# Optimization experiments

Measured on AMD Instinct MI355X. Metric: run time of the kernel, lower is better.

The kernel has to match this reference:

```python
import jax, jax.numpy as jnp
import numpy as np

NEG_INF = jnp.float32(-(2.0**32) + 1.0)


def squash(z):
    # z: [B, k_max, out_units]
    sq_norm = jnp.sum(jnp.square(z), axis=-1, keepdims=True)
    scale = sq_norm / (1.0 + sq_norm) / jnp.sqrt(sq_norm + 1e-8)
    return scale * z


def setup_inputs() -> dict:
    key = jax.random.key(0)
    k1, k2, k3, k4 = jax.random.split(key, 4)
    B, L, D_IN, D_OUT, K = 1024, 200, 256, 256, 8
    behavior_embeddings = jax.random.normal(k1, (B, L, D_IN), dtype=jnp.float32)
    seq_len = jax.random.randint(k2, (B, 1), 1, L + 1, dtype=jnp.int32)
    routing_logits = jax.random.normal(k3, (1, K, L), dtype=jnp.float32)  # init_std=1.0
    bilinear_mapping_matrix = jax.random.normal(k4, (D_IN, D_OUT), dtype=jnp.float32)
    return {
        "behavior_embeddings": behavior_embeddings,
        "seq_len": seq_len,
        "routing_logits": routing_logits,
        "bilinear_mapping_matrix": bilinear_mapping_matrix,
    }


def reference(behavior_embeddings, seq_len, routing_logits, bilinear_mapping_matrix):
    ITERATION_TIMES = 3
    B, L, _ = behavior_embeddings.shape
    K = routing_logits.shape[1]

    # mask: [B, 1, L] broadcastable to [B, K, L] (same seq_len for every capsule)
    mask = jnp.arange(L)[None, None, :] < seq_len[:, :, None]

    # bilinear map is loop-invariant: [B, L, out_units]
    mapped = jnp.einsum("ble,eo->blo", behavior_embeddings, bilinear_mapping_matrix)

    logits = routing_logits  # [1, K, L]
    interest_capsules = None
    for _ in range(ITERATION_TIMES):
        logits_pad = jnp.where(mask, jnp.broadcast_to(logits, (B, K, L)), NEG_INF)
        weight = jax.nn.softmax(logits_pad, axis=-1)          # [B, K, L]
        Z = jnp.einsum("bkl,blo->bko", weight, mapped)         # [B, K, out]
        interest_capsules = squash(Z)                          # [B, K, out]
        # delta: sum over batch of capsules @ mapped^T -> [1, K, L]
        delta = jnp.einsum("bko,blo->kl", interest_capsules, mapped)[None]
        logits = logits + delta  # emulates assign_add on non-trainable B

    return interest_capsules.reshape(-1, K, interest_capsules.shape[-1])
```

## Files before the change

kernel.cpp:

```cpp
#include <hip/hip_runtime.h>
#include <cstdint>
#include <cstddef>

#define B_    1024
#define L_    200
#define DIN_  256
#define DOUT_ 256
#define K_    8
#define M_    (B_ * L_)

typedef __attribute__((ext_vector_type(8))) short bf16x8;
typedef __attribute__((ext_vector_type(4))) float f32x4;

__device__ __forceinline__ float bf2f(unsigned short u) {
  union { unsigned int i; float f; } w; w.i = ((unsigned int)u) << 16; return w.f;
}
__device__ __forceinline__ unsigned short f2bf(float f) {
  union { float f; unsigned int i; } w; w.f = f;
  unsigned int x = w.i;
  return (unsigned short)((x + 0x7fffu + ((x >> 16) & 1u)) >> 16);
}

__device__ __forceinline__ void gload16(const void* g, void* l) {
  __builtin_amdgcn_global_load_lds(
      (const __attribute__((address_space(1))) unsigned int*)g,
      (__attribute__((address_space(3))) unsigned int*)l, 16, 0, 0);
}

__global__ __launch_bounds__(256)
void wt_prep(const float* __restrict__ W, unsigned short* __restrict__ Wh,
             unsigned short* __restrict__ Wm, unsigned short* __restrict__ Wl)
{
  const int k = blockIdx.x;
  const int n = threadIdx.x;
  float x = W[k * DOUT_ + n];
  unsigned short h = f2bf(x);
  float r = x - bf2f(h);
  unsigned short m = f2bf(r);
  float r2 = r - bf2f(m);
  unsigned short l = f2bf(r2);
  const int k0b = k >> 5, quad = (k >> 3) & 3, j = k & 7;
  const int nt = n >> 4, lr = n & 15;
  const size_t idx = ((((size_t)k0b * 16 + nt) * 64) + (quad * 16 + lr)) * 8 + j;
  Wh[idx] = h;
  Wm[idx] = m;
  Wl[idx] = l;
}

__global__ __launch_bounds__(256, 3)
void gemm_mapped(const float* __restrict__ A,
                 const unsigned short* __restrict__ Wh,
                 const unsigned short* __restrict__ Wm,
                 const unsigned short* __restrict__ Wl,
                 float* __restrict__ C)
{
  const int t    = threadIdx.x;
  const int wave = t >> 6;
  const int lane = t & 63;
  const int quad = lane >> 4;
  const int lr   = lane & 15;
  const int m0   = blockIdx.x * 64 + (wave & 1) * 32;
  const int nt0  = (wave >> 1) * 8;

  __shared__ unsigned short ldsB[3 * 16 * 64 * 8];

  f32x4 acc[2][8];
  #pragma unroll
  for (int mt = 0; mt < 2; ++mt)
    #pragma unroll
    for (int nt = 0; nt < 8; ++nt)
      acc[mt][nt] = (f32x4){0.f, 0.f, 0.f, 0.f};

  bf16x8 ah[2], am[2], al[2];
  float4 Af[2][2];

  const float* ap0 = A + (size_t)(m0 + lr) * DIN_ + quad * 8;
  const float* ap1 = A + (size_t)(m0 + 16 + lr) * DIN_ + quad * 8;

#define STAGE(K0B) do { \
    const size_t _k = (size_t)(K0B) * 8192; \
    _Pragma("unroll") \
    for (int _r = 0; _r < 4; ++_r) { \
      gload16(Wh + _k + _r * 2048 + t * 8, ldsB +         _r * 2048 + t * 8); \
      gload16(Wm + _k + _r * 2048 + t * 8, ldsB +  8192 + _r * 2048 + t * 8); \
      gload16(Wl + _k + _r * 2048 + t * 8, ldsB + 16384 + _r * 2048 + t * 8); \
    } \
  } while (0)

  Af[0][0] = *(const float4*)(ap0);
  Af[0][1] = *(const float4*)(ap0 + 4);
  Af[1][0] = *(const float4*)(ap1);
  Af[1][1] = *(const float4*)(ap1 + 4);
  STAGE(0);
  asm volatile("s_waitcnt vmcnt(0)" ::: "memory");
  __syncthreads();

  for (int k0b = 0; k0b < 8; ++k0b) {
    #pragma unroll
    for (int mt = 0; mt < 2; ++mt) {
      float xs[8] = {Af[mt][0].x, Af[mt][0].y, Af[mt][0].z, Af[mt][0].w,
                     Af[mt][1].x, Af[mt][1].y, Af[mt][1].z, Af[mt][1].w};
      #pragma unroll
      for (int j = 0; j < 8; ++j) {
        unsigned short h = f2bf(xs[j]);
        float r = xs[j] - bf2f(h);
        unsigned short mm = f2bf(r);
        float r2 = r - bf2f(mm);
        unsigned short ll = f2bf(r2);
        ah[mt][j] = (short)h; am[mt][j] = (short)mm; al[mt][j] = (short)ll;
      }
    }
    if (k0b < 7) {
      const int ko = (k0b + 1) * 32;
      Af[0][0] = *(const float4*)(ap0 + ko);
      Af[0][1] = *(const float4*)(ap0 + ko + 4);
      Af[1][0] = *(const float4*)(ap1 + ko);
      Af[1][1] = *(const float4*)(ap1 + ko + 4);
    }

#define GROUP(NT) do { \
    const unsigned short* _lb = ldsB + (size_t)((nt0 + (NT)) * 64 + lane) * 8; \
    bf16x8 Bh_ = *(const bf16x8*)(_lb); \
    bf16x8 Bm_ = *(const bf16x8*)(_lb + 8192); \
    bf16x8 Bl_ = *(const bf16x8*)(_lb + 16384); \
    f32x4 c0 = acc[0][NT], c1 = acc[1][NT]; \
    c0 = __builtin_amdgcn_mfma_f32_16x16x32_bf16(ah[0], Bh_, c0, 0, 0, 0); \
    c1 = __builtin_amdgcn_mfma_f32_16x16x32_bf16(ah[1], Bh_, c1, 0, 0, 0); \
    c0 = __builtin_amdgcn_mfma_f32_16x16x32_bf16(ah[0], Bm_, c0, 0, 0, 0); \
    c1 = __builtin_amdgcn_mfma_f32_16x16x32_bf16(ah[1], Bm_, c1, 0, 0, 0); \
    c0 = __builtin_amdgcn_mfma_f32_16x16x32_bf16(am[0], Bh_, c0, 0, 0, 0); \
    c1 = __builtin_amdgcn_mfma_f32_16x16x32_bf16(am[1], Bh_, c1, 0, 0, 0); \
    c0 = __builtin_amdgcn_mfma_f32_16x16x32_bf16(ah[0], Bl_, c0, 0, 0, 0); \
    c1 = __builtin_amdgcn_mfma_f32_16x16x32_bf16(ah[1], Bl_, c1, 0, 0, 0); \
    c0 = __builtin_amdgcn_mfma_f32_16x16x32_bf16(am[0], Bm_, c0, 0, 0, 0); \
    c1 = __builtin_amdgcn_mfma_f32_16x16x32_bf16(am[1], Bm_, c1, 0, 0, 0); \
    c0 = __builtin_amdgcn_mfma_f32_16x16x32_bf16(al[0], Bh_, c0, 0, 0, 0); \
    c1 = __builtin_amdgcn_mfma_f32_16x16x32_bf16(al[1], Bh_, c1, 0, 0, 0); \
    acc[0][NT] = c0; acc[1][NT] = c1; \
  } while (0)

    GROUP(0); GROUP(1); GROUP(2); GROUP(3);
    GROUP(4); GROUP(5); GROUP(6); GROUP(7);
#undef GROUP

    __syncthreads();
    if (k0b < 7) {
      STAGE(k0b + 1);
      asm volatile("s_waitcnt vmcnt(0)" ::: "memory");
      __syncthreads();
    }
  }
#undef STAGE

  #pragma unroll
  for (int mt = 0; mt < 2; ++mt)
    #pragma unroll
    for (int nt = 0; nt < 8; ++nt)
      #pragma unroll
      for (int r = 0; r < 4; ++r) {
        int row = m0 + mt * 16 + quad * 4 + r;
        C[(size_t)row * DOUT_ + (nt0 + nt) * 16 + lr] = acc[mt][nt][r];
      }
}

#define DSCALE     67108864.0f
#define DSCALE_INV 1.4901161193847656e-8f

__global__ __launch_bounds__(256, 4)
void z_soft(const float* __restrict__ mapped,
            const float* __restrict__ rlog,
            const long long* __restrict__ accA,
            const long long* __restrict__ accB,
            const int* __restrict__ seq_len,
            float* __restrict__ caps)
{
  const int t    = threadIdx.x;
  const int lane = t & 63;
  const int wave = t >> 6;
  const int b    = blockIdx.x;
  const int len  = seq_len[b];

  __shared__ float wsmT[200][8];
  __shared__ float zred[2][8][256];
  __shared__ float sqred[4][8];

  #pragma unroll
  for (int kk = 0; kk < 2; ++kk) {
    const int k = wave * 2 + kk;
    float v[4];
    float mx = -3.4028235e38f;
    #pragma unroll
    for (int i = 0; i < 4; ++i) {
      int l = lane + 64 * i;
      float lv = -3.4028235e38f;
      if (l < len) {
        long long a = accA[(k * L_ + l) * 8] + accB[(k * L_ + l) * 8];
        lv = rlog[k * L_ + l] + (float)a * DSCALE_INV;
      }
      v[i] = lv;
      mx = fmaxf(mx, lv);
    }
    #pragma unroll
    for (int s = 1; s < 64; s <<= 1) mx = fmaxf(mx, __shfl_xor(mx, s, 64));
    float e[4]; float sum = 0.f;
    #pragma unroll
    for (int i = 0; i < 4; ++i) {
      int l = lane + 64 * i;
      e[i] = (l < len) ? __expf(v[i] - mx) : 0.f;
      sum += e[i];
    }
    #pragma unroll
    for (int s = 1; s < 64; s <<= 1) sum += __shfl_xor(sum, s, 64);
    float inv = 1.f / sum;
    #pragma unroll
    for (int i = 0; i < 4; ++i) {
      int l = lane + 64 * i;
      if (l < L_) wsmT[l][k] = e[i] * inv;
    }
  }
  __syncthreads();

  f32x4 zacc[K_];
  #pragma unroll
  for (int k = 0; k < K_; ++k) zacc[k] = (f32x4){0.f, 0.f, 0.f, 0.f};

  const float* mp = mapped + (size_t)b * (L_ * DOUT_) + lane * 4;
  for (int l = wave; l < len; l += 16) {
    int  li[4];
    bool vi[4];
    #pragma unroll
    for (int r = 0; r < 4; ++r) {
      int lr_ = l + 4 * r;
      vi[r] = (lr_ < L_);
      li[r] = vi[r] ? lr_ : (L_ - 1);
    }
    f32x4 m[4];
    #pragma unroll
    for (int r = 0; r < 4; ++r)
      m[r] = *(const f32x4*)(mp + (size_t)li[r] * DOUT_);
    #pragma unroll
    for (int r = 0; r < 4; ++r) {
      float4 w0 = *(const float4*)&wsmT[li[r]][0];
      float4 w1 = *(const float4*)&wsmT[li[r]][4];
      if (!vi[r]) {
        w0.x = w0.y = w0.z = w0.w = 0.f;
        w1.x = w1.y = w1.z = w1.w = 0.f;
      }
      zacc[0] += w0.x * m[r]; zacc[1] += w0.y * m[r];
      zacc[2] += w0.z * m[r]; zacc[3] += w0.w * m[r];
      zacc[4] += w1.x * m[r]; zacc[5] += w1.y * m[r];
      zacc[6] += w1.z * m[r]; zacc[7] += w1.w * m[r];
    }
  }

  if (wave >= 2) {
    #pragma unroll
    for (int k = 0; k < K_; ++k)
      *(f32x4*)&zred[wave - 2][k][lane * 4] = zacc[k];
  }
  __syncthreads();
  if (wave < 2) {
    #pragma unroll
    for (int k = 0; k < K_; ++k) {
      f32x4 r = *(const f32x4*)&zred[wave][k][lane * 4];
      r += zacc[k];
      *(f32x4*)&zred[wave][k][lane * 4] = r;
    }
  }
  __syncthreads();

  float z[K_];
  #pragma unroll
  for (int k = 0; k < K_; ++k) z[k] = zred[0][k][t] + zred[1][k][t];

  #pragma unroll
  for (int k = 0; k < K_; ++k) {
    float s2 = z[k] * z[k];
    #pragma unroll
    for (int s = 1; s < 64; s <<= 1) s2 += __shfl_xor(s2, s, 64);
    if (lane == 0) sqred[wave][k] = s2;
  }
  __syncthreads();
  #pragma unroll
  for (int k = 0; k < K_; ++k) {
    float sq = sqred[0][k] + sqred[1][k] + sqred[2][k] + sqred[3][k];
    float scale = sq / ((1.f + sq) * sqrtf(sq + 1e-8f));
    caps[((size_t)b * K_ + k) * DOUT_ + t] = scale * z[k];
  }
}

__global__ __launch_bounds__(256)
void delta_kernel(const float* __restrict__ mapped, const float* __restrict__ caps,
                  long long* __restrict__ accOut)
{
  const int t    = threadIdx.x;
  const int lane = t & 63;
  const int wave = t >> 6;
  const int wid  = blockIdx.x * 4 + wave;
  const int lc   = wid % 50;
  const int bc   = wid / 50;
  const int l0   = lc * 4;
  const int o4   = lane * 4;

  const float* cb = caps   + (size_t)(bc * 16) * (K_ * DOUT_) + o4;
  const float* mb = mapped + ((size_t)(bc * 16) * L_ + l0) * DOUT_ + o4;

  float acc[K_][4];
  #pragma unroll
  for (int k = 0; k < K_; ++k)
    #pragma unroll
    for (int ll = 0; ll < 4; ++ll) acc[k][ll] = 0.f;

  float4 cA[K_], mA[4], cB[K_], mB[4];

#define LOADC(DST, BI) do { \
    const float* _p = cb + (size_t)(BI) * (K_ * DOUT_); \
    _Pragma("unroll") \
    for (int _k = 0; _k < K_; ++_k) DST[_k] = *(const float4*)(_p + _k * DOUT_); \
  } while (0)
#define LOADM(DST, BI) do { \
    const float* _p = mb + (size_t)(BI) * (L_ * DOUT_); \
    _Pragma("unroll") \
    for (int _l = 0; _l < 4; ++_l) DST[_l] = *(const float4*)(_p + _l * DOUT_); \
  } while (0)
#define COMPUTE(CC, MM) do { \
    _Pragma("unroll") \
    for (int _k = 0; _k < K_; ++_k) \
      _Pragma("unroll") \
      for (int _l = 0; _l < 4; ++_l) \
        acc[_k][_l] += CC[_k].x * MM[_l].x + CC[_k].y * MM[_l].y \
                     + CC[_k].z * MM[_l].z + CC[_k].w * MM[_l].w; \
  } while (0)

  LOADC(cA, 0); LOADM(mA, 0);
  for (int i = 0; i < 8; ++i) {
    LOADC(cB, 2 * i + 1); LOADM(mB, 2 * i + 1);
    COMPUTE(cA, mA);
    if (i < 7) { LOADC(cA, 2 * i + 2); LOADM(mA, 2 * i + 2); }
    COMPUTE(cB, mB);
  }
#undef LOADC
#undef LOADM
#undef COMPUTE

  float out = 0.f;
  #pragma unroll
  for (int k = 0; k < K_; ++k)
    #pragma unroll
    for (int ll = 0; ll < 4; ++ll) {
      float v = acc[k][ll];
      v += __shfl_xor(v, 1, 64);
      v += __shfl_xor(v, 2, 64);
      v += __shfl_xor(v, 4, 64);
      v += __shfl_xor(v, 8, 64);
      v += __shfl_xor(v, 16, 64);
      v += __shfl_xor(v, 32, 64);
      if (lane == k * 4 + ll) out = v;
    }
  if (lane < 32) {
    long long q = llrintf(out * DSCALE);
    atomicAdd((unsigned long long*)&accOut[((size_t)(lane >> 2) * L_ + l0 + (lane & 3)) * 8],
              (unsigned long long)q);
  }
}

__global__ __launch_bounds__(256)
void init_acc(long long* __restrict__ a)
{
  int i = blockIdx.x * 256 + threadIdx.x;
  a[i] = 0;
}

extern "C" void kernel_launch(void* const* d_in, const int* in_sizes, int n_in,
                              void* d_out, int out_size, void* d_ws, size_t ws_size,
                              hipStream_t stream)
{
  const float* behav = (const float*)d_in[0];
  const int*   slen  = (const int*)d_in[1];
  const float* rlog  = (const float*)d_in[2];
  const float* W     = (const float*)d_in[3];
  float* caps = (float*)d_out;

  char* ws = (char*)d_ws;
  long long* z0   = (long long*)ws;
  long long* acc0 = (long long*)(ws + 102400);
  long long* acc1 = (long long*)(ws + 204800);
  unsigned short* Wh = (unsigned short*)(ws + 327680);
  unsigned short* Wm = (unsigned short*)(ws + 458752);
  unsigned short* Wl = (unsigned short*)(ws + 589824);
  float* mapped   = (float*)(ws + (1 << 20));

  init_acc<<<dim3(150), 256, 0, stream>>>((long long*)ws);
  wt_prep<<<dim3(256), 256, 0, stream>>>(W, Wh, Wm, Wl);
  gemm_mapped<<<dim3(3200), 256, 0, stream>>>(behav, Wh, Wm, Wl, mapped);

  z_soft<<<dim3(B_), 256, 0, stream>>>(mapped, rlog, z0,   z0,   slen, caps);
  delta_kernel<<<dim3(800), 256, 0, stream>>>(mapped, caps, acc0);
  z_soft<<<dim3(B_), 256, 0, stream>>>(mapped, rlog, acc0, z0,   slen, caps);
  delta_kernel<<<dim3(800), 256, 0, stream>>>(mapped, caps, acc1);
  z_soft<<<dim3(B_), 256, 0, stream>>>(mapped, rlog, acc0, acc1, slen, caps);
}
```

Baseline: 556.8 us.

## Software-pipeline bilinear GEMM with split-half LDS staging and fine-grained vmcnt waits

Restructures the bf16x3 split GEMM main loop into an unrolled software pipeline. The B tile load is split into two halves, and the next step's first half is issued while the second half of the MFMA groups runs. A operands are double-buffered two k-steps ahead. Full vmcnt(0) waits plus syncthreads are replaced with partial vmcnt counts and raw s_barrier, so global-to-LDS loads overlap compute instead of stalling each k-step. The cost is more registers and fragile hand-counted vmcnt and barrier ordering.

Result: slower. 830.3 us (+49.1%).

```diff
diff --git a/kernel.cpp b/kernel.cpp
--- a/kernel.cpp
+++ b/kernel.cpp
@@ -72,51 +72,46 @@
       acc[mt][nt] = (f32x4){0.f, 0.f, 0.f, 0.f};
 
   bf16x8 ah[2], am[2], al[2];
-  float4 Af[2][2];
+  float4 Af0[2][2], Af1[2][2];
 
   const float* ap0 = A + (size_t)(m0 + lr) * DIN_ + quad * 8;
   const float* ap1 = A + (size_t)(m0 + 16 + lr) * DIN_ + quad * 8;
 
-#define STAGE(K0B) do { \
-    const size_t _k = (size_t)(K0B) * 8192; \
+#define STAGE_H(K0B, H) do { \
+    const size_t _g = (size_t)(K0B) * 8192 + (H) * 2048 + t * 8; \
+    const int    _l = (H) * 2048 + t * 8; \
+    gload16(Wh + _g,        ldsB + _l); \
+    gload16(Wh + _g + 4096, ldsB + _l + 4096); \
+    gload16(Wm + _g,        ldsB + 8192 + _l); \
+    gload16(Wm + _g + 4096, ldsB + 8192 + _l + 4096); \
+    gload16(Wl + _g,        ldsB + 16384 + _l); \
+    gload16(Wl + _g + 4096, ldsB + 16384 + _l + 4096); \
+  } while (0)
+
+#define ISSUE_A(K0B, AF) do { \
+    const int _ko = (K0B) * 32; \
+    AF[0][0] = *(const float4*)(ap0 + _ko); \
+    AF[0][1] = *(const float4*)(ap0 + _ko + 4); \
+    AF[1][0] = *(const float4*)(ap1 + _ko); \
+    AF[1][1] = *(const float4*)(ap1 + _ko + 4); \
+  } while (0)
+
+#define CONVERT(AF) do { \
     _Pragma("unroll") \
-    for (int _r = 0; _r < 4; ++_r) { \
-      gload16(Wh + _k + _r * 2048 + t * 8, ldsB +         _r * 2048 + t * 8); \
-      gload16(Wm + _k + _r * 2048 + t * 8, ldsB +  8192 + _r * 2048 + t * 8); \
-      gload16(Wl + _k + _r * 2048 + t * 8, ldsB + 16384 + _r * 2048 + t * 8); \
+    for (int mt = 0; mt < 2; ++mt) { \
+      float xs[8] = {AF[mt][0].x, AF[mt][0].y, AF[mt][0].z, AF[mt][0].w, \
+                     AF[mt][1].x, AF[mt][1].y, AF[mt][1].z, AF[mt][1].w}; \
+      _Pragma("unroll") \
+      for (int j = 0; j < 8; ++j) { \
+        unsigned short h = f2bf(xs[j]); \
+        float r = xs[j] - bf2f(h); \
+        unsigned short mm = f2bf(r); \
+        float r2 = r - bf2f(mm); \
+        unsigned short ll = f2bf(r2); \
+        ah[mt][j] = (short)h; am[mt][j] = (short)mm; al[mt][j] = (short)ll; \
+      } \
     } \
   } while (0)
-
-  Af[0][0] = *(const float4*)(ap0);
-  Af[0][1] = *(const float4*)(ap0 + 4);
-  Af[1][0] = *(const float4*)(ap1);
-  Af[1][1] = *(const float4*)(ap1 + 4);
-  STAGE(0);
-  asm volatile("s_waitcnt vmcnt(0)" ::: "memory");
-  __syncthreads();
-
-  for (int k0b = 0; k0b < 8; ++k0b) {
-    #pragma unroll
-    for (int mt = 0; mt < 2; ++mt) {
-      float xs[8] = {Af[mt][0].x, Af[mt][0].y, Af[mt][0].z, Af[mt][0].w,
-                     Af[mt][1].x, Af[mt][1].y, Af[mt][1].z, Af[mt][1].w};
-      #pragma unroll
-      for (int j = 0; j < 8; ++j) {
-        unsigned short h = f2bf(xs[j]);
-        float r = xs[j] - bf2f(h);
-        unsigned short mm = f2bf(r);
-        float r2 = r - bf2f(mm);
-        unsigned short ll = f2bf(r2);
-        ah[mt][j] = (short)h; am[mt][j] = (short)mm; al[mt][j] = (short)ll;
-      }
-    }
-    if (k0b < 7) {
-      const int ko = (k0b + 1) * 32;
-      Af[0][0] = *(const float4*)(ap0 + ko);
-      Af[0][1] = *(const float4*)(ap0 + ko + 4);
-      Af[1][0] = *(const float4*)(ap1 + ko);
-      Af[1][1] = *(const float4*)(ap1 + ko + 4);
-    }
 
 #define GROUP(NT) do { \
     const unsigned short* _lb = ldsB + (size_t)((nt0 + (NT)) * 64 + lane) * 8; \
@@ -139,18 +134,52 @@
     acc[0][NT] = c0; acc[1][NT] = c1; \
   } while (0)
 
-    GROUP(0); GROUP(1); GROUP(2); GROUP(3);
-    GROUP(4); GROUP(5); GROUP(6); GROUP(7);
+#define WAITV(N) asm volatile("s_waitcnt vmcnt(" #N ")" ::: "memory")
+#define BAR() do { __builtin_amdgcn_s_barrier(); __builtin_amdgcn_sched_barrier(0); } while (0)
+
+#define KSTEP_FULL(K, AF) do { \
+    WAITV(10); BAR(); \
+    CONVERT(AF); \
+    GROUP(0); GROUP(1); GROUP(2); GROUP(3); \
+    WAITV(4); BAR(); \
+    STAGE_H((K) + 1, 0); \
+    GROUP(4); GROUP(5); GROUP(6); GROUP(7); \
+    BAR(); \
+    STAGE_H((K) + 1, 1); \
+    ISSUE_A((K) + 2, AF); \
+  } while (0)
+
+  ISSUE_A(0, Af0);
+  STAGE_H(0, 0);
+  STAGE_H(0, 1);
+  ISSUE_A(1, Af1);
+
+  for (int kk = 0; kk < 3; ++kk) {
+    const int k = kk * 2;
+    KSTEP_FULL(k, Af0);
+    KSTEP_FULL(k + 1, Af1);
+  }
+  WAITV(10); BAR();
+  CONVERT(Af0);
+  GROUP(0); GROUP(1); GROUP(2); GROUP(3);
+  WAITV(4); BAR();
+  STAGE_H(7, 0);
+  GROUP(4); GROUP(5); GROUP(6); GROUP(7);
+  BAR();
+  STAGE_H(7, 1);
+  WAITV(6); BAR();
+  CONVERT(Af1);
+  GROUP(0); GROUP(1); GROUP(2); GROUP(3);
+  WAITV(0); BAR();
+  GROUP(4); GROUP(5); GROUP(6); GROUP(7);
+
+#undef KSTEP_FULL
+#undef WAITV
+#undef BAR
 #undef GROUP
-
-    __syncthreads();
-    if (k0b < 7) {
-      STAGE(k0b + 1);
-      asm volatile("s_waitcnt vmcnt(0)" ::: "memory");
-      __syncthreads();
-    }
-  }
-#undef STAGE
+#undef CONVERT
+#undef ISSUE_A
+#undef STAGE_H
 
   #pragma unroll
   for (int mt = 0; mt < 2; ++mt)
```
